# Kernel tuning notes

Hardware: AMD Instinct MI355X
Metric: run time of the kernel (lower is better)

The kernel has to match this reference:

```python
import jax, jax.numpy as jnp
import numpy as np

BLOCK = 192
SCALE = 2048 ** (-0.5)


def setup_inputs() -> dict:
    key = jax.random.key(0)
    k1, k2, k3, k4 = jax.random.split(key, 4)
    B, N, C = 8, 1920, 512
    x = jax.random.normal(k1, (B, N, C), dtype=jnp.float32)
    g = jax.random.normal(k2, (B, N, C), dtype=jnp.float32)
    # nn.Linear(dim, dim, bias=False) weights, stored as [out, in] like torch
    Wq = jax.random.normal(k3, (C, C), dtype=jnp.float32) * (1.0 / np.sqrt(C))
    Wg = jax.random.normal(k4, (C, C), dtype=jnp.float32) * (1.0 / np.sqrt(C))
    return {"x": x, "g": g, "Wq": Wq, "Wg": Wg}


def reference(x, g, Wq, Wg):
    B, N, C = g.shape
    # q = x + mean over tokens of g
    q = x + jnp.mean(g, axis=1, keepdims=True)
    rel_q = jnp.einsum('bnc,dc->bnd', q, Wq)  # Linear: y = x @ W^T
    # ---- block-local cosine attention over chunks of 192 tokens ----
    gb = g.reshape(B * N // BLOCK, BLOCK, C)
    norm = jnp.linalg.norm(gb, axis=-1, keepdims=True)
    rel = gb / jnp.maximum(norm, 1e-12)  # F.normalize(dim=-1)
    scores = jnp.einsum('bic,bjc->bij', rel, rel) * SCALE  # [nb,192,192]
    attn = jax.nn.softmax(scores, axis=-1)
    g2 = jnp.einsum('bij,bjc->bic', attn, gb).reshape(B, N, C)
    # ---- global cross attention ----
    rel_g = jnp.einsum('bnc,dc->bnd', g2, Wg)
    scores2 = jnp.einsum('bmc,bnc->bmn', rel_q, rel_g) * SCALE  # [B,M,N]
    attn2 = jax.nn.softmax(scores2, axis=-1)
    out = jnp.einsum('bmn,bnc->bmc', attn2, g2)
    return out
```

## Files before the change

kernel.cpp:

```cpp
#include <hip/hip_runtime.h>
#include <math.h>

constexpr int Bsz  = 8;
constexpr int Ntok = 1920;
constexpr int Cdim = 512;
constexpr int BLK  = 192;
constexpr int Mrows = Bsz * Ntok;
constexpr int NBLK  = Mrows / BLK;
constexpr float SCALE = 0.02209708691207961f;

typedef _Float16 half8 __attribute__((ext_vector_type(8)));
typedef float    f32x4 __attribute__((ext_vector_type(4)));

#define GLOAD_LDS16(gp, lp) __builtin_amdgcn_global_load_lds( \
    (const __attribute__((address_space(1))) void*)(gp),      \
    (__attribute__((address_space(3))) void*)(lp), 16, 0, 0)

__device__ inline unsigned short f2h(float f) {
    _Float16 h = (_Float16)f;
    return __builtin_bit_cast(unsigned short, h);
}
__device__ inline float h2f(unsigned short u) {
    return (float)__builtin_bit_cast(_Float16, u);
}

template<int BK> __device__ inline int smask(int r) {
    return (BK == 32) ? ((r & 3) ^ ((r >> 2) & 3)) : (r & 7);
}

template<int N> __device__ __forceinline__ void vm_wait() {
    if constexpr (N == 0)      asm volatile("s_waitcnt vmcnt(0)" ::: "memory");
    else if constexpr (N == 2) asm volatile("s_waitcnt vmcnt(2)" ::: "memory");
    else if constexpr (N == 4) asm volatile("s_waitcnt vmcnt(4)" ::: "memory");
    else if constexpr (N == 6) asm volatile("s_waitcnt vmcnt(6)" ::: "memory");
    else                       asm volatile("s_waitcnt vmcnt(8)" ::: "memory");
}

__global__ __launch_bounds__(256) void prep_g(
    const float* __restrict__ g, unsigned short* __restrict__ gh,
    float* __restrict__ invn)
{
    int wid = threadIdx.x >> 6, lane = threadIdx.x & 63;
    int row = blockIdx.x * 4 + wid;
    const float* p = g + (size_t)row * Cdim + lane * 8;
    float4 v0 = *(const float4*)p;
    float4 v1 = *(const float4*)(p + 4);
    float ss = v0.x * v0.x + v0.y * v0.y + v0.z * v0.z + v0.w * v0.w
             + v1.x * v1.x + v1.y * v1.y + v1.z * v1.z + v1.w * v1.w;
    #pragma unroll
    for (int o = 1; o < 64; o <<= 1) ss += __shfl_xor(ss, o);
    if (lane == 0) invn[row] = 1.0f / fmaxf(sqrtf(ss), 1e-12f);
    ushort4 h0, h1;
    h0.x = f2h(v0.x); h0.y = f2h(v0.y); h0.z = f2h(v0.z); h0.w = f2h(v0.w);
    h1.x = f2h(v1.x); h1.y = f2h(v1.y); h1.z = f2h(v1.z); h1.w = f2h(v1.w);
    ushort4* d = (ushort4*)(gh + (size_t)row * Cdim + lane * 8);
    d[0] = h0; d[1] = h1;
}

__global__ void mean_partial(const unsigned short* __restrict__ gh, float* __restrict__ part) {
    int b = blockIdx.x, t = blockIdx.y, c = threadIdx.x;
    const unsigned short* p = gh + ((size_t)b * Ntok + (size_t)t * 48) * Cdim + c;
    float s = 0.f;
    #pragma unroll 4
    for (int n = 0; n < 48; ++n) s += h2f(p[(size_t)n * Cdim]);
    part[((size_t)b * 40 + t) * Cdim + c] = s;
}

__global__ void mean_final(const float* __restrict__ part, float* __restrict__ meang) {
    int b = blockIdx.x, c = threadIdx.x;
    float s = 0.f;
    for (int t = 0; t < 40; ++t) s += part[((size_t)b * 40 + t) * Cdim + c];
    meang[b * Cdim + c] = s * (1.0f / (float)Ntok);
}

__global__ void cvt_k(const float* __restrict__ src, const float* __restrict__ bias,
                      unsigned short* __restrict__ dst, int n4) {
    int i = blockIdx.x * 256 + threadIdx.x;
    if (i >= n4) return;
    float4 v = ((const float4*)src)[i];
    if (bias) {
        int b  = i / (Ntok * Cdim / 4);
        int c4 = (i & (Cdim / 4 - 1)) << 2;
        float4 bv = *(const float4*)&bias[b * Cdim + c4];
        v.x += bv.x; v.y += bv.y; v.z += bv.z; v.w += bv.w;
    }
    ushort4 h;
    h.x = f2h(v.x); h.y = f2h(v.y); h.z = f2h(v.z); h.w = f2h(v.w);
    ((ushort4*)dst)[i] = h;
}

__global__ __launch_bounds__(256) void transpose1(
    const unsigned short* __restrict__ in, unsigned short* __restrict__ out,
    int R, int C, long inB, long outB)
{
    int z = blockIdx.z;
    in  += (size_t)z * inB;
    out += (size_t)z * outB;
    __shared__ unsigned short th[64][68];
    int r0 = blockIdx.y * 64, c0 = blockIdx.x * 64;
    int tr = threadIdx.x >> 4, tc = (threadIdx.x & 15) * 4;
    for (int rr = tr; rr < 64; rr += 16) {
        ushort4 h = *(const ushort4*)&in[(size_t)(r0 + rr) * C + c0 + tc];
        th[tc + 0][rr] = h.x; th[tc + 1][rr] = h.y; th[tc + 2][rr] = h.z; th[tc + 3][rr] = h.w;
    }
    __syncthreads();
    for (int cc = tr; cc < 64; cc += 16) {
        ushort4 h = *(const ushort4*)&th[cc][tc];
        *(ushort4*)&out[(size_t)(c0 + cc) * R + r0 + tc] = h;
    }
}

template<int FM, int FN, int BK>
__global__ __launch_bounds__(256) void mfma_gemm(
    const unsigned short* __restrict__ A, const unsigned short* __restrict__ B,
    float* __restrict__ Of32, unsigned short* __restrict__ Oh,
    int N, int K, int ld,
    long aB, long bB, long oB,
    float alpha, const float* __restrict__ rs, const float* __restrict__ cs, int sB)
{
    constexpr int BM = FM * 32, BN = FN * 32;
    constexpr int RPC = 512 / BK;
    constexpr int LPR = BK / 8;
    constexpr int NCH = (BM + BN) / RPC;
    constexpr int CPW = NCH / 4;
    int z = blockIdx.z;

    int gx = gridDim.x;
    int nwg = gx * gridDim.y;
    int orig = blockIdx.y * gx + blockIdx.x;
    int q = nwg >> 3, r = nwg & 7;
    int xcd = orig & 7, idx = orig >> 3;
    int wgid = (xcd < r ? xcd * (q + 1) : r * (q + 1) + (xcd - r) * q) + idx;
    int m0 = (wgid / gx) * BM, n0 = (wgid % gx) * BN;

    __shared__ __align__(16) unsigned short As[2][BM * BK];
    __shared__ __align__(16) unsigned short Bs[2][BN * BK];

    int tid  = threadIdx.x;
    int lane = tid & 63, wid = tid >> 6;
    int wm = (wid >> 1) * (FM * 16), wn = (wid & 1) * (FN * 16);

    int srow = lane / LPR;
    int sgc  = (lane % LPR) ^ smask<BK>(srow);

    const unsigned short* csrc[CPW];
    unsigned short* cdst0[CPW];
    unsigned short* cdst1[CPW];
    #pragma unroll
    for (int i = 0; i < CPW; ++i) {
        int c = wid * CPW + i;
        if (c < BM / RPC) {
            csrc[i]  = A + (size_t)z * aB + (size_t)(m0 + c * RPC + srow) * ld + sgc * 8;
            cdst0[i] = &As[0][c * 512];
            cdst1[i] = &As[1][c * 512];
        } else {
            int cb = c - BM / RPC;
            csrc[i]  = B + (size_t)z * bB + (size_t)(n0 + cb * RPC + srow) * ld + sgc * 8;
            cdst0[i] = &Bs[0][cb * 512];
            cdst1[i] = &Bs[1][cb * 512];
        }
    }

    f32x4 acc[FM][FN] = {};
    int fr = lane & 15, kq = lane >> 4;

    const int nt = K / BK;
    #pragma unroll
    for (int i = 0; i < CPW; ++i) GLOAD_LDS16(csrc[i], cdst0[i]);
    #pragma unroll
    for (int i = 0; i < CPW; ++i) GLOAD_LDS16(csrc[i] + BK, cdst1[i]);

    for (int t = 0; t < nt; ++t) {
        int cur = t & 1;
        if (t + 1 < nt) vm_wait<CPW>(); else vm_wait<0>();
        __builtin_amdgcn_sched_barrier(0);
        __builtin_amdgcn_s_barrier();
        __builtin_amdgcn_sched_barrier(0);

        const unsigned short* Ab = As[cur];
        const unsigned short* Bb = Bs[cur];
        #pragma unroll
        for (int ks = 0; ks < BK / 32; ++ks) {
            int slot = ks * 4 + kq;
            half8 a[FM], b[FN];
            #pragma unroll
            for (int f = 0; f < FM; ++f) {
                int rr = wm + f * 16 + fr;
                a[f] = *(const half8*)&Ab[rr * BK + ((slot ^ smask<BK>(rr)) << 3)];
            }
            #pragma unroll
            for (int f = 0; f < FN; ++f) {
                int rr = wn + f * 16 + fr;
                b[f] = *(const half8*)&Bb[rr * BK + ((slot ^ smask<BK>(rr)) << 3)];
            }
            #pragma unroll
            for (int i = 0; i < FM; ++i)
                #pragma unroll
                for (int j = 0; j < FN; ++j)
                    acc[i][j] = __builtin_amdgcn_mfma_f32_16x16x32_f16(a[i], b[j], acc[i][j], 0, 0, 0);
        }

        __builtin_amdgcn_sched_barrier(0);
        __builtin_amdgcn_s_barrier();
        if (t + 2 < nt) {
            const int k2 = (t + 2) * BK;
            #pragma unroll
            for (int i = 0; i < CPW; ++i)
                GLOAD_LDS16(csrc[i] + k2, cur ? cdst1[i] : cdst0[i]);
        }
    }

    float* O          = Of32 ? Of32 + (size_t)z * oB : nullptr;
    unsigned short* H = Oh   ? Oh   + (size_t)z * oB : nullptr;
    int fq = lane >> 4;
    #pragma unroll
    for (int i = 0; i < FM; ++i) {
        #pragma unroll
        for (int r4 = 0; r4 < 4; ++r4) {
            int gm = m0 + wm + i * 16 + fq * 4 + r4;
            float rf = alpha * (rs ? rs[(size_t)z * sB + gm] : 1.0f);
            #pragma unroll
            for (int j = 0; j < FN; ++j) {
                int gn = n0 + wn + j * 16 + fr;
                float v = acc[i][j][r4] * rf * (cs ? cs[(size_t)z * sB + gn] : 1.0f);
                size_t off = (size_t)gm * N + gn;
                if (O) O[off] = v;
                else   H[off] = f2h(v);
            }
        }
    }
}

__global__ __launch_bounds__(512, 2) void gemm256(
    const unsigned short* __restrict__ A, const unsigned short* __restrict__ B,
    unsigned short* __restrict__ Oh, float* __restrict__ psum,
    int M, int N, int K, int ld,
    long aB, long bB, long oB, float alpha)
{
    int z = blockIdx.z;
    int gx = gridDim.x;
    int nwg = gx * gridDim.y;
    int orig = blockIdx.y * gx + blockIdx.x;
    int q = nwg >> 3, r = nwg & 7;
    int xcd = orig & 7, idx = orig >> 3;
    int wgid = (xcd < r ? xcd * (q + 1) : r * (q + 1) + (xcd - r) * q) + idx;
    int bx = wgid % gx;
    int m0 = (wgid / gx) * 256, n0 = bx * 256;

    __shared__ __align__(16) unsigned short As[2][256 * 64];
    __shared__ __align__(16) unsigned short Bs[2][256 * 64];

    int tid = threadIdx.x, lane = tid & 63, wid = tid >> 6;
    int wr = wid >> 2, wc = wid & 3;
    const unsigned short* Az = A + (size_t)z * aB;
    const unsigned short* Bz = B + (size_t)z * bB;

    int srow8 = lane >> 3;
    int sslot = (lane & 7) ^ srow8;

    auto stageT = [&](int t) {
        int cur = t & 1;
        const int koff = t * 64;
        #pragma unroll
        for (int i = 0; i < 4; ++i) {
            int c = wid * 4 + i;
            int rrow = c * 8 + srow8;
            int gr = min(m0 + rrow, M - 1);
            GLOAD_LDS16(Az + (size_t)gr * ld + koff + sslot * 8, &As[cur][c * 512]);
        }
        #pragma unroll
        for (int i = 0; i < 4; ++i) {
            int c = wid * 4 + i;
            int rrow = c * 8 + srow8;
            int gc = min(n0 + rrow, N - 1);
            GLOAD_LDS16(Bz + (size_t)gc * ld + koff + sslot * 8, &Bs[cur][c * 512]);
        }
    };

    f32x4 acc[8][4] = {};
    int fr = lane & 15, kq = lane >> 4;

    const int nt = K / 64;
    stageT(0);
    stageT(1);

    for (int t = 0; t < nt; ++t) {
        int cur = t & 1;
        if (t + 1 < nt) vm_wait<8>(); else vm_wait<0>();
        __builtin_amdgcn_sched_barrier(0);
        __builtin_amdgcn_s_barrier();
        __builtin_amdgcn_sched_barrier(0);

        const unsigned short* Ab = As[cur];
        const unsigned short* Bb = Bs[cur];
        __builtin_amdgcn_s_setprio(1);
        half8 b[4][2];
        #pragma unroll
        for (int nf = 0; nf < 4; ++nf) {
            int rr = wc * 64 + nf * 16 + fr;
            #pragma unroll
            for (int ks = 0; ks < 2; ++ks) {
                int slot = (ks * 4 + kq) ^ (rr & 7);
                b[nf][ks] = *(const half8*)&Bb[rr * 64 + slot * 8];
            }
        }
        #pragma unroll
        for (int mf = 0; mf < 8; ++mf) {
            int rr = wr * 128 + mf * 16 + fr;
            half8 a[2];
            #pragma unroll
            for (int ks = 0; ks < 2; ++ks) {
                int slot = (ks * 4 + kq) ^ (rr & 7);
                a[ks] = *(const half8*)&Ab[rr * 64 + slot * 8];
            }
            #pragma unroll
            for (int nf = 0; nf < 4; ++nf)
                #pragma unroll
                for (int ks = 0; ks < 2; ++ks)
                    acc[mf][nf] = __builtin_amdgcn_mfma_f32_16x16x32_f16(
                        a[ks], b[nf][ks], acc[mf][nf], 0, 0, 0);
        }
        __builtin_amdgcn_s_setprio(0);

        __builtin_amdgcn_sched_barrier(0);
        __builtin_amdgcn_s_barrier();
        __builtin_amdgcn_sched_barrier(0);
        if (t + 2 < nt) stageT(t + 2);
    }

    unsigned short* H = Oh + (size_t)z * oB;
    int fq = lane >> 4;
    #pragma unroll
    for (int mi = 0; mi < 8; ++mi) {
        #pragma unroll
        for (int r4 = 0; r4 < 4; ++r4) {
            int gm = m0 + wr * 128 + mi * 16 + fq * 4 + r4;
            bool vrow = gm < M;
            float rsum = 0.f;
            #pragma unroll
            for (int ni = 0; ni < 4; ++ni) {
                int gn = n0 + wc * 64 + ni * 16 + fr;
                float e = __expf(acc[mi][ni][r4] * alpha);
                if (vrow && gn < N) {
                    H[(size_t)gm * N + gn] = f2h(e);
                    rsum += e;
                }
            }
            rsum += __shfl_xor(rsum, 1);
            rsum += __shfl_xor(rsum, 2);
            rsum += __shfl_xor(rsum, 4);
            rsum += __shfl_xor(rsum, 8);
            if (vrow && fr == 0)
                psum[((size_t)z * M + gm) * 32 + bx * 4 + wc] = rsum;
        }
    }
}

__global__ void rowsum_inv(const float* __restrict__ ps, float* __restrict__ inv, int rows) {
    int i = blockIdx.x * 256 + threadIdx.x;
    if (i >= rows) return;
    const float* p = ps + (size_t)i * 32;
    float s = 0.f;
    #pragma unroll
    for (int j = 0; j < 32; ++j) s += p[j];
    inv[i] = 1.0f / s;
}

__global__ __launch_bounds__(256) void softmax_h(unsigned short* __restrict__ P, int cols) {
    __shared__ float buf[1920];
    __shared__ float red[4];
    size_t row = blockIdx.x;
    unsigned short* p = P + row * (size_t)cols;
    int tid = threadIdx.x;
    int nq = cols >> 2;

    float lmax = -1e30f;
    for (int q = tid; q < nq; q += 256) {
        ushort4 h = ((const ushort4*)p)[q];
        float v0 = h2f(h.x), v1 = h2f(h.y), v2 = h2f(h.z), v3 = h2f(h.w);
        buf[q * 4 + 0] = v0; buf[q * 4 + 1] = v1;
        buf[q * 4 + 2] = v2; buf[q * 4 + 3] = v3;
        lmax = fmaxf(lmax, fmaxf(fmaxf(v0, v1), fmaxf(v2, v3)));
    }
    #pragma unroll
    for (int o = 1; o < 64; o <<= 1) lmax = fmaxf(lmax, __shfl_xor(lmax, o));
    if ((tid & 63) == 0) red[tid >> 6] = lmax;
    __syncthreads();
    float bmax = fmaxf(fmaxf(red[0], red[1]), fmaxf(red[2], red[3]));

    float lsum = 0.f;
    for (int c = tid; c < cols; c += 256) {
        float e = expf(buf[c] - bmax);
        buf[c] = e;
        lsum += e;
    }
    #pragma unroll
    for (int o = 1; o < 64; o <<= 1) lsum += __shfl_xor(lsum, o);
    __syncthreads();
    if ((tid & 63) == 0) red[tid >> 6] = lsum;
    __syncthreads();
    float inv = 1.0f / (red[0] + red[1] + red[2] + red[3]);

    for (int q = tid; q < nq; q += 256) {
        ushort4 h;
        h.x = f2h(buf[q * 4 + 0] * inv);
        h.y = f2h(buf[q * 4 + 1] * inv);
        h.z = f2h(buf[q * 4 + 2] * inv);
        h.w = f2h(buf[q * 4 + 3] * inv);
        ((ushort4*)p)[q] = h;
    }
}

extern "C" void kernel_launch(void* const* d_in, const int* in_sizes, int n_in,
                              void* d_out, int out_size, void* d_ws, size_t ws_size,
                              hipStream_t stream) {
    (void)in_sizes; (void)n_in; (void)out_size; (void)ws_size;
    const float* x  = (const float*)d_in[0];
    const float* g  = (const float*)d_in[1];
    const float* Wq = (const float*)d_in[2];
    const float* Wg = (const float*)d_in[3];
    float* out = (float*)d_out;

    const size_t GE = (size_t)Mrows * Cdim;
    char* ws = (char*)d_ws;
    size_t off = 0;
    auto alloc = [&](size_t bytes) { char* p = ws + off; off += (bytes + 255) & ~(size_t)255; return p; };

    float* meang = (float*)alloc(Bsz * Cdim * 4);
    float* part  = (float*)alloc(Bsz * 40 * Cdim * 4);
    float* invn  = (float*)alloc(Mrows * 4);
    unsigned short* gh   = (unsigned short*)alloc(GE * 2);
    unsigned short* gTh  = (unsigned short*)alloc(GE * 2);
    unsigned short* qh   = (unsigned short*)alloc(GE * 2);
    unsigned short* wqh  = (unsigned short*)alloc((size_t)Cdim * Cdim * 2);
    unsigned short* wgh  = (unsigned short*)alloc((size_t)Cdim * Cdim * 2);
    unsigned short* rqh  = (unsigned short*)alloc(GE * 2);
    unsigned short* rgh  = (unsigned short*)alloc(GE * 2);
    unsigned short* g2h  = (unsigned short*)alloc(GE * 2);
    unsigned short* sbh  = (unsigned short*)alloc((size_t)NBLK * BLK * BLK * 2);
    unsigned short* s2h  = (unsigned short*)alloc((size_t)Bsz * Ntok * Ntok * 2);
    float* psum  = (float*)alloc((size_t)Mrows * 32 * 4);
    float* rsinv = (float*)alloc((size_t)Mrows * 4);
    unsigned short* g2Th = qh;

    prep_g<<<Mrows / 4, 256, 0, stream>>>(g, gh, invn);

    mean_partial<<<dim3(Bsz, 40), 512, 0, stream>>>(gh, part);
    mean_final<<<Bsz, 512, 0, stream>>>(part, meang);

    cvt_k<<<(int)(GE / 4 + 255) / 256, 256, 0, stream>>>(x, meang, qh, (int)(GE / 4));
    cvt_k<<<(Cdim * Cdim / 4) / 256, 256, 0, stream>>>(Wq, nullptr, wqh, Cdim * Cdim / 4);
    cvt_k<<<(Cdim * Cdim / 4) / 256, 256, 0, stream>>>(Wg, nullptr, wgh, Cdim * Cdim / 4);

    transpose1<<<dim3(Cdim / 64, BLK / 64, NBLK), 256, 0, stream>>>(
        gh, gTh, BLK, Cdim, (long)BLK * Cdim, (long)Cdim * BLK);

    mfma_gemm<2, 4, 64><<<dim3(Cdim / 128, Mrows / 64), 256, 0, stream>>>(
        qh, wqh, nullptr, rqh, Cdim, Cdim, Cdim, 0, 0, 0, 1.0f, nullptr, nullptr, 0);

    mfma_gemm<2, 2, 32><<<dim3(3, 3, NBLK), 256, 0, stream>>>(
        gh, gh, nullptr, sbh, BLK, Cdim, Cdim,
        (long)BLK * Cdim, (long)BLK * Cdim, (long)BLK * BLK,
        SCALE, invn, invn, BLK);

    softmax_h<<<NBLK * BLK, 256, 0, stream>>>(sbh, BLK);

    mfma_gemm<2, 4, 64><<<dim3(Cdim / 128, BLK / 64, NBLK), 256, 0, stream>>>(
        sbh, gTh, nullptr, g2h, Cdim, BLK, BLK,
        (long)BLK * BLK, (long)Cdim * BLK, (long)BLK * Cdim,
        1.0f, nullptr, nullptr, 0);

    transpose1<<<dim3(Cdim / 64, Ntok / 64, Bsz), 256, 0, stream>>>(
        g2h, g2Th, Ntok, Cdim, (long)Ntok * Cdim, (long)Cdim * Ntok);

    mfma_gemm<2, 4, 64><<<dim3(Cdim / 128, Mrows / 64), 256, 0, stream>>>(
        g2h, wgh, nullptr, rgh, Cdim, Cdim, Cdim, 0, 0, 0, 1.0f, nullptr, nullptr, 0);

    gemm256<<<dim3(8, 8, Bsz), 512, 0, stream>>>(
        rqh, rgh, s2h, psum, Ntok, Ntok, Cdim, Cdim,
        (long)Ntok * Cdim, (long)Ntok * Cdim, (long)Ntok * Ntok, SCALE);

    rowsum_inv<<<(Mrows + 255) / 256, 256, 0, stream>>>(psum, rsinv, Mrows);

    mfma_gemm<4, 4, 64><<<dim3(Cdim / 128, Ntok / 128, Bsz), 256, 0, stream>>>(
        s2h, g2Th, out, nullptr, Cdim, Ntok, Ntok,
        (long)Ntok * Ntok, (long)Cdim * Ntok, (long)Ntok * Cdim,
        1.0f, rsinv, nullptr, Ntok);
}
```

Before: 233.3 us.

## Fold weight products into one matrix and fuse block softmax into score GEMM

The two projections are reassociated: Wq and Wg are combined once into a single 512x512 matrix (Wg^T·Wq), and q is multiplied by it, so the global score GEMM runs directly against g2. This removes one full token-by-channel GEMM and the rel_g buffer. The block-local softmax kernel is dropped. The block score GEMM epilogue now exponentiates scores and writes per-slot row sums, and the following attention-times-values GEMM applies the reciprocal as a row scale. Softmax without max subtraction relies on cosine scores being bounded, and the reassociated product changes fp16 rounding.

```diff
diff --git a/kernel.cpp b/kernel.cpp
--- a/kernel.cpp
+++ b/kernel.cpp
@@ -116,7 +116,8 @@
     float* __restrict__ Of32, unsigned short* __restrict__ Oh,
     int N, int K, int ld,
     long aB, long bB, long oB,
-    float alpha, const float* __restrict__ rs, const float* __restrict__ cs, int sB)
+    float alpha, const float* __restrict__ rs, const float* __restrict__ cs, int sB,
+    float* __restrict__ psum, int pM, int pSlots)
 {
     constexpr int BM = FM * 32, BN = FN * 32;
     constexpr int RPC = 512 / BK;
@@ -131,7 +132,8 @@
     int q = nwg >> 3, r = nwg & 7;
     int xcd = orig & 7, idx = orig >> 3;
     int wgid = (xcd < r ? xcd * (q + 1) : r * (q + 1) + (xcd - r) * q) + idx;
-    int m0 = (wgid / gx) * BM, n0 = (wgid % gx) * BN;
+    int bx = wgid % gx;
+    int m0 = (wgid / gx) * BM, n0 = bx * BN;
 
     __shared__ __align__(16) unsigned short As[2][BM * BK];
     __shared__ __align__(16) unsigned short Bs[2][BN * BK];
@@ -213,19 +215,46 @@
     float* O          = Of32 ? Of32 + (size_t)z * oB : nullptr;
     unsigned short* H = Oh   ? Oh   + (size_t)z * oB : nullptr;
     int fq = lane >> 4;
-    #pragma unroll
-    for (int i = 0; i < FM; ++i) {
-        #pragma unroll
-        for (int r4 = 0; r4 < 4; ++r4) {
-            int gm = m0 + wm + i * 16 + fq * 4 + r4;
-            float rf = alpha * (rs ? rs[(size_t)z * sB + gm] : 1.0f);
-            #pragma unroll
-            for (int j = 0; j < FN; ++j) {
-                int gn = n0 + wn + j * 16 + fr;
-                float v = acc[i][j][r4] * rf * (cs ? cs[(size_t)z * sB + gn] : 1.0f);
-                size_t off = (size_t)gm * N + gn;
-                if (O) O[off] = v;
-                else   H[off] = f2h(v);
+    if (psum) {
+        int slotB = bx * (BN / 32) + (wn >> 5);
+        #pragma unroll
+        for (int i = 0; i < FM; ++i) {
+            #pragma unroll
+            for (int r4 = 0; r4 < 4; ++r4) {
+                int gm = m0 + wm + i * 16 + fq * 4 + r4;
+                float rf = alpha * (rs ? rs[(size_t)z * sB + gm] : 1.0f);
+                float rsum = 0.f;
+                #pragma unroll
+                for (int j = 0; j < FN; ++j) {
+                    int gn = n0 + wn + j * 16 + fr;
+                    float v = acc[i][j][r4] * rf * (cs ? cs[(size_t)z * sB + gn] : 1.0f);
+                    float e = __expf(v);
+                    H[(size_t)gm * N + gn] = f2h(e);
+                    rsum += e;
+                }
+                rsum += __shfl_xor(rsum, 1);
+                rsum += __shfl_xor(rsum, 2);
+                rsum += __shfl_xor(rsum, 4);
+                rsum += __shfl_xor(rsum, 8);
+                if (fr == 0)
+                    psum[((size_t)z * pM + gm) * pSlots + slotB] = rsum;
+            }
+        }
+    } else {
+        #pragma unroll
+        for (int i = 0; i < FM; ++i) {
+            #pragma unroll
+            for (int r4 = 0; r4 < 4; ++r4) {
+                int gm = m0 + wm + i * 16 + fq * 4 + r4;
+                float rf = alpha * (rs ? rs[(size_t)z * sB + gm] : 1.0f);
+                #pragma unroll
+                for (int j = 0; j < FN; ++j) {
+                    int gn = n0 + wn + j * 16 + fr;
+                    float v = acc[i][j][r4] * rf * (cs ? cs[(size_t)z * sB + gn] : 1.0f);
+                    size_t off = (size_t)gm * N + gn;
+                    if (O) O[off] = v;
+                    else   H[off] = f2h(v);
+                }
             }
         }
     }
@@ -356,59 +385,14 @@
     }
 }
 
-__global__ void rowsum_inv(const float* __restrict__ ps, float* __restrict__ inv, int rows) {
+__global__ void rowsum_inv(const float* __restrict__ ps, float* __restrict__ inv,
+                           int rows, int slots) {
     int i = blockIdx.x * 256 + threadIdx.x;
     if (i >= rows) return;
-    const float* p = ps + (size_t)i * 32;
+    const float* p = ps + (size_t)i * slots;
     float s = 0.f;
-    #pragma unroll
-    for (int j = 0; j < 32; ++j) s += p[j];
+    for (int j = 0; j < slots; ++j) s += p[j];
     inv[i] = 1.0f / s;
-}
-
-__global__ __launch_bounds__(256) void softmax_h(unsigned short* __restrict__ P, int cols) {
-    __shared__ float buf[1920];
-    __shared__ float red[4];
-    size_t row = blockIdx.x;
-    unsigned short* p = P + row * (size_t)cols;
-    int tid = threadIdx.x;
-    int nq = cols >> 2;
-
-    float lmax = -1e30f;
-    for (int q = tid; q < nq; q += 256) {
-        ushort4 h = ((const ushort4*)p)[q];
-        float v0 = h2f(h.x), v1 = h2f(h.y), v2 = h2f(h.z), v3 = h2f(h.w);
-        buf[q * 4 + 0] = v0; buf[q * 4 + 1] = v1;
-        buf[q * 4 + 2] = v2; buf[q * 4 + 3] = v3;
-        lmax = fmaxf(lmax, fmaxf(fmaxf(v0, v1), fmaxf(v2, v3)));
-    }
-    #pragma unroll
-    for (int o = 1; o < 64; o <<= 1) lmax = fmaxf(lmax, __shfl_xor(lmax, o));
-    if ((tid & 63) == 0) red[tid >> 6] = lmax;
-    __syncthreads();
-    float bmax = fmaxf(fmaxf(red[0], red[1]), fmaxf(red[2], red[3]));
-
-    float lsum = 0.f;
-    for (int c = tid; c < cols; c += 256) {
-        float e = expf(buf[c] - bmax);
-        buf[c] = e;
-        lsum += e;
-    }
-    #pragma unroll
-    for (int o = 1; o < 64; o <<= 1) lsum += __shfl_xor(lsum, o);
-    __syncthreads();
-    if ((tid & 63) == 0) red[tid >> 6] = lsum;
-    __syncthreads();
-    float inv = 1.0f / (red[0] + red[1] + red[2] + red[3]);
-
-    for (int q = tid; q < nq; q += 256) {
-        ushort4 h;
-        h.x = f2h(buf[q * 4 + 0] * inv);
-        h.y = f2h(buf[q * 4 + 1] * inv);
-        h.z = f2h(buf[q * 4 + 2] * inv);
-        h.w = f2h(buf[q * 4 + 3] * inv);
-        ((ushort4*)p)[q] = h;
-    }
 }
 
 extern "C" void kernel_launch(void* const* d_in, const int* in_sizes, int n_in,
@@ -422,6 +406,7 @@
     float* out = (float*)d_out;
 
     const size_t GE = (size_t)Mrows * Cdim;
+    const size_t WE = (size_t)Cdim * Cdim;
     char* ws = (char*)d_ws;
     size_t off = 0;
     auto alloc = [&](size_t bytes) { char* p = ws + off; off += (bytes + 255) & ~(size_t)255; return p; };
@@ -432,15 +417,19 @@
     unsigned short* gh   = (unsigned short*)alloc(GE * 2);
     unsigned short* gTh  = (unsigned short*)alloc(GE * 2);
     unsigned short* qh   = (unsigned short*)alloc(GE * 2);
-    unsigned short* wqh  = (unsigned short*)alloc((size_t)Cdim * Cdim * 2);
-    unsigned short* wgh  = (unsigned short*)alloc((size_t)Cdim * Cdim * 2);
-    unsigned short* rqh  = (unsigned short*)alloc(GE * 2);
-    unsigned short* rgh  = (unsigned short*)alloc(GE * 2);
+    unsigned short* wqh  = (unsigned short*)alloc(WE * 2);
+    unsigned short* wgh  = (unsigned short*)alloc(WE * 2);
+    unsigned short* wqT  = (unsigned short*)alloc(WE * 2);
+    unsigned short* wgT  = (unsigned short*)alloc(WE * 2);
+    unsigned short* wh   = (unsigned short*)alloc(WE * 2);
+    unsigned short* qWh  = (unsigned short*)alloc(GE * 2);
     unsigned short* g2h  = (unsigned short*)alloc(GE * 2);
     unsigned short* sbh  = (unsigned short*)alloc((size_t)NBLK * BLK * BLK * 2);
     unsigned short* s2h  = (unsigned short*)alloc((size_t)Bsz * Ntok * Ntok * 2);
-    float* psum  = (float*)alloc((size_t)Mrows * 32 * 4);
-    float* rsinv = (float*)alloc((size_t)Mrows * 4);
+    float* psum   = (float*)alloc((size_t)Mrows * 32 * 4);
+    float* psumb  = (float*)alloc((size_t)Mrows * 6 * 4);
+    float* rsinv  = (float*)alloc((size_t)Mrows * 4);
+    float* rsinvb = (float*)alloc((size_t)Mrows * 4);
     unsigned short* g2Th = qh;
 
     prep_g<<<Mrows / 4, 256, 0, stream>>>(g, gh, invn);
@@ -449,41 +438,45 @@
     mean_final<<<Bsz, 512, 0, stream>>>(part, meang);
 
     cvt_k<<<(int)(GE / 4 + 255) / 256, 256, 0, stream>>>(x, meang, qh, (int)(GE / 4));
-    cvt_k<<<(Cdim * Cdim / 4) / 256, 256, 0, stream>>>(Wq, nullptr, wqh, Cdim * Cdim / 4);
-    cvt_k<<<(Cdim * Cdim / 4) / 256, 256, 0, stream>>>(Wg, nullptr, wgh, Cdim * Cdim / 4);
+    cvt_k<<<(int)(WE / 4) / 256, 256, 0, stream>>>(Wq, nullptr, wqh, (int)(WE / 4));
+    cvt_k<<<(int)(WE / 4) / 256, 256, 0, stream>>>(Wg, nullptr, wgh, (int)(WE / 4));
+    transpose1<<<dim3(8, 8, 1), 256, 0, stream>>>(wqh, wqT, Cdim, Cdim, 0, 0);
+    transpose1<<<dim3(8, 8, 1), 256, 0, stream>>>(wgh, wgT, Cdim, Cdim, 0, 0);
+
+    mfma_gemm<2, 2, 64><<<dim3(8, 8), 256, 0, stream>>>(
+        wgT, wqT, nullptr, wh, Cdim, Cdim, Cdim, 0, 0, 0,
+        1.0f, nullptr, nullptr, 0, nullptr, 0, 0);
 
     transpose1<<<dim3(Cdim / 64, BLK / 64, NBLK), 256, 0, stream>>>(
         gh, gTh, BLK, Cdim, (long)BLK * Cdim, (long)Cdim * BLK);
 
     mfma_gemm<2, 4, 64><<<dim3(Cdim / 128, Mrows / 64), 256, 0, stream>>>(
-        qh, wqh, nullptr, rqh, Cdim, Cdim, Cdim, 0, 0, 0, 1.0f, nullptr, nullptr, 0);
+        qh, wh, nullptr, qWh, Cdim, Cdim, Cdim, 0, 0, 0,
+        1.0f, nullptr, nullptr, 0, nullptr, 0, 0);
 
     mfma_gemm<2, 2, 32><<<dim3(3, 3, NBLK), 256, 0, stream>>>(
         gh, gh, nullptr, sbh, BLK, Cdim, Cdim,
         (long)BLK * Cdim, (long)BLK * Cdim, (long)BLK * BLK,
-        SCALE, invn, invn, BLK);
-
-    softmax_h<<<NBLK * BLK, 256, 0, stream>>>(sbh, BLK);
+        SCALE, invn, invn, BLK, psumb, BLK, 6);
+
+    rowsum_inv<<<(Mrows + 255) / 256, 256, 0, stream>>>(psumb, rsinvb, Mrows, 6);
 
     mfma_gemm<2, 4, 64><<<dim3(Cdim / 128, BLK / 64, NBLK), 256, 0, stream>>>(
         sbh, gTh, nullptr, g2h, Cdim, BLK, BLK,
         (long)BLK * BLK, (long)Cdim * BLK, (long)BLK * Cdim,
-        1.0f, nullptr, nullptr, 0);
+        1.0f, rsinvb, nullptr, BLK, nullptr, 0, 0);
 
     transpose1<<<dim3(Cdim / 64, Ntok / 64, Bsz), 256, 0, stream>>>(
         g2h, g2Th, Ntok, Cdim, (long)Ntok * Cdim, (long)Cdim * Ntok);
 
-    mfma_gemm<2, 4, 64><<<dim3(Cdim / 128, Mrows / 64), 256, 0, stream>>>(
-        g2h, wgh, nullptr, rgh, Cdim, Cdim, Cdim, 0, 0, 0, 1.0f, nullptr, nullptr, 0);
-
     gemm256<<<dim3(8, 8, Bsz), 512, 0, stream>>>(
-        rqh, rgh, s2h, psum, Ntok, Ntok, Cdim, Cdim,
+        qWh, g2h, s2h, psum, Ntok, Ntok, Cdim, Cdim,
         (long)Ntok * Cdim, (long)Ntok * Cdim, (long)Ntok * Ntok, SCALE);
 
-    rowsum_inv<<<(Mrows + 255) / 256, 256, 0, stream>>>(psum, rsinv, Mrows);
+    rowsum_inv<<<(Mrows + 255) / 256, 256, 0, stream>>>(psum, rsinv, Mrows, 32);
 
     mfma_gemm<4, 4, 64><<<dim3(Cdim / 128, Ntok / 128, Bsz), 256, 0, stream>>>(
         s2h, g2Th, out, nullptr, Cdim, Ntok, Ntok,
         (long)Ntok * Ntok, (long)Cdim * Ntok, (long)Ntok * Cdim,
-        1.0f, rsinv, nullptr, Ntok);
-}
+        1.0f, rsinv, nullptr, Ntok, nullptr, 0, 0);
+}
```

New measurement: 221.5 us. -5.0%, faster.
